# Kernel tuning notes

Measured on AMD Instinct MI355X. Metric: run time of the kernel, lower is better.

Reference implementation:

```python
import jax, jax.numpy as jnp
import numpy as np

EPS = 1e-12  # torch F.normalize eps

def _l2norm(t):
    # normalize over last axis (tokens N), matching F.normalize(dim=-1)
    n = jnp.sqrt(jnp.sum(t * t, axis=-1, keepdims=True))
    return t / jnp.maximum(n, EPS)

def setup_inputs() -> dict:
    key = jax.random.key(0)
    ks = jax.random.split(key, 4)
    B, N, C, H = 16, 3136, 768, 16
    x = jax.random.normal(ks[0], (B, N, C), dtype=jnp.float32)
    w_qkv = jax.random.normal(ks[1], (3 * C, C), dtype=jnp.float32) * (C ** -0.5)
    temperature = jnp.ones((H, 1, 1), dtype=jnp.float32)
    w_proj = jax.random.normal(ks[2], (C, C), dtype=jnp.float32) * (C ** -0.5)
    b_proj = jnp.zeros((C,), dtype=jnp.float32)
    return {"x": x, "w_qkv": w_qkv, "temperature": temperature,
            "w_proj": w_proj, "b_proj": b_proj}

def reference(x, w_qkv, temperature, w_proj, b_proj):
    B, N, C = x.shape
    H = temperature.shape[0]
    dh = C // H
    # qkv: [B,N,3C] -> [B,N,3,H,dh] -> [3,B,H,dh,N]
    qkv = (x @ w_qkv.T).reshape(B, N, 3, H, dh)
    qkv = jnp.transpose(qkv, (2, 0, 3, 4, 1))
    q, k, v = qkv[0], qkv[1], qkv[2]          # each [B,H,dh,N]
    q = _l2norm(q)
    k = _l2norm(k)
    # cross-covariance attention over channel axis: [B,H,dh,dh]
    attn = jnp.einsum('bhdn,bhen->bhde', q, k) * temperature
    attn = jax.nn.softmax(attn, axis=-1)
    out = jnp.einsum('bhde,bhen->bhdn', attn, v)  # [B,H,dh,N]
    out = jnp.transpose(out, (0, 3, 1, 2)).reshape(B, N, C)
    return out @ w_proj.T + b_proj
```

## Files before the change

kernel.cpp:

```cpp
#include <hip/hip_runtime.h>
#include <hip/hip_bf16.h>
#include <stdint.h>

using f32x4   = __attribute__((ext_vector_type(4))) float;
using half8   = __attribute__((ext_vector_type(8))) _Float16;
using half4   = __attribute__((ext_vector_type(4))) _Float16;
using half2v  = __attribute__((ext_vector_type(2))) _Float16;
using float4v = __attribute__((ext_vector_type(4))) float;

typedef const __attribute__((address_space(1))) void gas_void;
typedef __attribute__((address_space(3))) void las_void;

__device__ __forceinline__ void gload_lds16(const void* gptr, void* lptr) {
  __builtin_amdgcn_global_load_lds((gas_void*)(uintptr_t)gptr,
                                   (las_void*)(uintptr_t)lptr, 16, 0, 0);
}

#define MFMA_F16(a, b, c) __builtin_amdgcn_mfma_f32_16x16x32_f16((a), (b), (c), 0, 0, 0)

__global__ __launch_bounds__(256)
void k_cvtx(const float* __restrict__ x, _Float16* __restrict__ x16,
            _Float16* __restrict__ xT,
            const float* __restrict__ wqkv, const float* __restrict__ wproj,
            _Float16* __restrict__ w16, _Float16* __restrict__ wp16,
            _Float16* __restrict__ wvT) {
  const int bid = blockIdx.x;
  if (bid >= 9408) {
    const long N1 = 221184L, N2 = 73728L, N3 = 98304L;
    const long total = N1 + N2 + N3;
    for (long i = (long)(bid - 9408) * blockDim.x + threadIdx.x; i < total;
         i += 512L * blockDim.x) {
      if (i < N1 + N2) {
        const float* src; _Float16* dst; long off;
        if (i < N1) { src = wqkv;  dst = w16;  off = i; }
        else        { src = wproj; dst = wp16; off = i - N1; }
        const float4v* p = (const float4v*)(src + off * 8);
        float4v a = p[0], b = p[1];
        half8 o;
        o[0] = (_Float16)a[0]; o[1] = (_Float16)a[1]; o[2] = (_Float16)a[2]; o[3] = (_Float16)a[3];
        o[4] = (_Float16)b[0]; o[5] = (_Float16)b[1]; o[6] = (_Float16)b[2]; o[7] = (_Float16)b[3];
        *(half8*)(dst + off * 8) = o;
      } else {
        const long u = i - N1 - N2;
        const int h = (int)(u / 6144);
        const int r = (int)(u % 6144);
        const int f = r >> 3, e0 = (r & 7) * 8;
        half8 o;
        if (e0 >= 48) {
#pragma unroll
          for (int j = 0; j < 8; ++j) o[j] = (_Float16)0.f;
        } else {
#pragma unroll
          for (int j = 0; j < 8; ++j)
            o[j] = (_Float16)wqkv[(long)(1536 + h * 48 + e0 + j) * 768 + f];
        }
        *(half8*)(wvT + ((long)(h * 768 + f) * 64 + e0)) = o;
      }
    }
    return;
  }
  __shared__ _Float16 lt[64 * 66];
  const int b = bid / 588;
  const int rem = bid % 588;
  const int tt = rem / 12, ct = rem % 12;
  const long t0g = (long)b * 3136 + tt * 64;
  const int c0 = ct * 64;
  const int tid = threadIdx.x;
#pragma unroll
  for (int ch = 0; ch < 4; ++ch) {
    const int idx = tid + ch * 256;
    const int tr = idx >> 4, cg = (idx & 15) * 4;
    float4v v = *(const float4v*)&x[(t0g + tr) * 768 + c0 + cg];
    half4 hv;
    hv[0] = (_Float16)v[0]; hv[1] = (_Float16)v[1];
    hv[2] = (_Float16)v[2]; hv[3] = (_Float16)v[3];
    *(half4*)&x16[(t0g + tr) * 768 + c0 + cg] = hv;
    half2v lo, hi;
    lo[0] = hv[0]; lo[1] = hv[1]; hi[0] = hv[2]; hi[1] = hv[3];
    *(half2v*)&lt[tr * 66 + cg]     = lo;
    *(half2v*)&lt[tr * 66 + cg + 2] = hi;
  }
  __syncthreads();
  const int c = tid >> 2, tch = tid & 3;
  half8 o0, o1;
#pragma unroll
  for (int j = 0; j < 8; ++j) o0[j] = lt[(tch * 16 + j) * 66 + c];
#pragma unroll
  for (int j = 0; j < 8; ++j) o1[j] = lt[(tch * 16 + 8 + j) * 66 + c];
  _Float16* dst = xT + (long)b * 2408448 + (long)(c0 + c) * 3136 + tt * 64 + tch * 16;
  *(half8*)dst = o0;
  *(half8*)(dst + 8) = o1;
}

__global__ __launch_bounds__(512)
void k_gram(const _Float16* __restrict__ xT, _Float16* __restrict__ G) {
  __shared__ _Float16 lds[2][2][128 * 64];
  const int tid = threadIdx.x;
  const int wv = tid >> 6, lane = tid & 63;
  const int g = lane >> 4, cidx = lane & 15;
  const int wr = wv >> 2, wc = wv & 3;

  const int nwg = (int)gridDim.x;
  const int q = nwg >> 3, r = nwg & 7;
  const int xcd = (int)blockIdx.x & 7, bidx = (int)blockIdx.x >> 3;
  int wg = (xcd < r ? xcd * (q + 1) : r * (q + 1) + (xcd - r) * q) + bidx;
  const int b = wg / 21;
  int p = wg % 21;
  int mt = 0;
  while (p >= 6 - mt) { p -= 6 - mt; ++mt; }
  const int nt = mt + p;

  const _Float16* Ab = xT + (long)b * 2408448 + (long)mt * 128 * 3136;
  const _Float16* Bb = xT + (long)b * 2408448 + (long)nt * 128 * 3136;

  const int srow8 = lane >> 3;
  const int sgr8  = (lane & 7) ^ srow8;

  auto stage = [&](int buf, int kt) {
#pragma unroll
    for (int l = 0; l < 2; ++l) {
      const int chunk = l * 8 + wv;
      const long grow = chunk * 8 + srow8;
      const long koff = (long)kt * 64 + sgr8 * 8;
      gload_lds16(Ab + grow * 3136 + koff, &lds[buf][0][chunk * 512]);
      gload_lds16(Bb + grow * 3136 + koff, &lds[buf][1][chunk * 512]);
    }
  };

  f32x4 acc[4][2] = {};
  stage(0, 0);
  __syncthreads();
  for (int kt = 0; kt < 49; ++kt) {
    const int cur = kt & 1;
    if (kt + 1 < 49) stage(cur ^ 1, kt + 1);
    half8 af[4][2], bf[2][2];
#pragma unroll
    for (int ks = 0; ks < 2; ++ks) {
      const int gran = (((ks << 2) + g) ^ (cidx & 7)) * 8;
#pragma unroll
      for (int m = 0; m < 4; ++m)
        af[m][ks] = *(const half8*)&lds[cur][0][(wr * 64 + m * 16 + cidx) * 64 + gran];
#pragma unroll
      for (int n = 0; n < 2; ++n)
        bf[n][ks] = *(const half8*)&lds[cur][1][(wc * 32 + n * 16 + cidx) * 64 + gran];
    }
#pragma unroll
    for (int ks = 0; ks < 2; ++ks)
#pragma unroll
      for (int m = 0; m < 4; ++m)
#pragma unroll
        for (int n = 0; n < 2; ++n)
          acc[m][n] = MFMA_F16(af[m][ks], bf[n][ks], acc[m][n]);
    __syncthreads();
  }
  _Float16* Gb = G + (long)b * 589824;
  const long m0 = (long)mt * 128, n0 = (long)nt * 128;
#pragma unroll
  for (int m = 0; m < 4; ++m)
#pragma unroll
    for (int rr = 0; rr < 4; ++rr) {
      const long row = m0 + wr * 64 + m * 16 + g * 4 + rr;
#pragma unroll
      for (int n = 0; n < 2; ++n)
        Gb[row * 768 + n0 + wc * 32 + n * 16 + cidx] = (_Float16)acc[m][n][rr];
    }
  if (mt != nt) {
#pragma unroll
    for (int m = 0; m < 4; ++m)
#pragma unroll
      for (int n = 0; n < 2; ++n) {
        half4 hv;
#pragma unroll
        for (int rr = 0; rr < 4; ++rr) hv[rr] = (_Float16)acc[m][n][rr];
        const long col  = n0 + wc * 32 + n * 16 + cidx;
        const long row0 = m0 + wr * 64 + m * 16 + g * 4;
        *(half4*)&Gb[col * 768 + row0] = hv;
      }
  }
}

#define XPH(CURA, CURB, MLO, NA, NBUF, NKS, NMLO, LOADB, NB, STAGE, BDRY)      \
  {                                                                            \
    STAGE;                                                                     \
    if (BDRY) {                                                                \
      asm volatile("s_waitcnt vmcnt(4)" ::: "memory");                         \
      __builtin_amdgcn_sched_barrier(0);                                       \
    }                                                                          \
    __builtin_amdgcn_s_barrier();                                              \
    _Pragma("unroll")                                                          \
    for (int mm = 0; mm < 4; ++mm)                                             \
      NA[mm] = *(const half8*)&lds[(NBUF)*32768 + (NKS)*8192 + raA + ((NMLO)+mm)*512]; \
    if (LOADB) {                                                               \
      _Pragma("unroll")                                                        \
      for (int nn = 0; nn < 4; ++nn)                                           \
        NB[nn] = *(const half8*)&lds[(NBUF)*32768 + (NKS)*8192 + raB + nn*512]; \
    }                                                                          \
    __builtin_amdgcn_sched_barrier(0);                                         \
    __builtin_amdgcn_s_setprio(1);                                             \
    _Pragma("unroll")                                                          \
    for (int mm = 0; mm < 4; ++mm)                                             \
      _Pragma("unroll")                                                        \
      for (int nn = 0; nn < 4; ++nn)                                           \
        acc[(MLO)+mm][nn] = MFMA_F16(CURA[mm], CURB[nn], acc[(MLO)+mm][nn]);   \
    __builtin_amdgcn_s_setprio(0);                                             \
    __builtin_amdgcn_s_barrier();                                              \
  }

template<bool OUT_F32>
__global__ __launch_bounds__(512, 2)
void k_gemm8p(const _Float16* __restrict__ A, const _Float16* __restrict__ B,
              void* __restrict__ Cv, const float* __restrict__ bias,
              int Mt, int Nt, long Areal, long Astr, long Bstr, long Cstr,
              long N, long K)
{
  __shared__ _Float16 lds[65536];
  const int tid  = threadIdx.x;
  const int wv   = tid >> 6, lane = tid & 63;
  const int g    = lane >> 4, cidx = lane & 15;
  const int wr   = wv >> 2, wc = wv & 3;

  const int nwg = (int)gridDim.x;
  const int q = nwg >> 3, r = nwg & 7;
  const int xcd = (int)blockIdx.x & 7, bidx = (int)blockIdx.x >> 3;
  int wg = (xcd < r ? xcd * (q + 1) : r * (q + 1) + (xcd - r) * q) + bidx;

  const int tpb = Mt * Nt;
  const int b   = wg / tpb;
  const int rem = wg - b * tpb;
  const long mt = rem % Mt, nt = rem / Mt;
  const long m0 = mt * 256, n0 = nt * 256;

  const int NT = (int)(K >> 6);
  const int NI = NT >> 1;

  const _Float16* Ab = A + b * Astr + m0 * K;
  const _Float16* Bb = B + b * Bstr + n0 * K;

  const int srow = lane >> 2;
  const int sgr  = (lane & 3) ^ ((lane >> 3) & 3);

  auto stage = [&](int op, int buf, int kh, int t) {
    const _Float16* src = op ? Bb : Ab;
    const long koff = (long)t * 64 + kh * 32 + sgr * 8;
#pragma unroll
    for (int l = 0; l < 2; ++l) {
      const int chunk = l * 8 + wv;
      gload_lds16(src + (long)(chunk * 16 + srow) * K + koff,
                  &lds[buf * 32768 + op * 16384 + kh * 8192 + chunk * 512]);
    }
  };

  const int gr  = (g ^ ((cidx >> 1) & 3)) * 8;
  const int raA = (wr * 128 + cidx) * 32 + gr;
  const int raB = 16384 + (wc * 64 + cidx) * 32 + gr;

  f32x4 acc[8][4] = {};

  stage(0, 0, 0, 0); stage(1, 0, 0, 0);
  stage(0, 0, 1, 0); stage(1, 0, 1, 0);
  stage(0, 1, 0, 1); stage(1, 1, 0, 1);
  asm volatile("s_waitcnt vmcnt(4)" ::: "memory");
  __builtin_amdgcn_sched_barrier(0);
  __builtin_amdgcn_s_barrier();

  half8 afA[4], afB[4], bfA[4], bfB[4];
#pragma unroll
  for (int mm = 0; mm < 4; ++mm) afA[mm] = *(const half8*)&lds[raA + mm * 512];
#pragma unroll
  for (int nn = 0; nn < 4; ++nn) bfA[nn] = *(const half8*)&lds[raB + nn * 512];

  for (int it = 0; it < NI; ++it) {
    const int t1c = 2 * it + 1;
    int tn2 = 2 * it + 2; if (tn2 >= NT) tn2 -= NT;
    int tn3 = 2 * it + 3; if (tn3 >= NT) tn3 -= NT;
    XPH(afA, bfA, 0, afB, 0, 0, 4, 0, bfB, stage(0, 1, 1, t1c), false)
    XPH(afB, bfA, 4, afA, 0, 1, 0, 1, bfB, stage(1, 1, 1, t1c), false)
    XPH(afA, bfB, 0, afB, 0, 1, 4, 0, bfA, stage(0, 0, 0, tn2), false)
    XPH(afB, bfB, 4, afA, 1, 0, 0, 1, bfA, stage(1, 0, 0, tn2), true )
    XPH(afA, bfA, 0, afB, 1, 0, 4, 0, bfB, stage(0, 0, 1, tn2), false)
    XPH(afB, bfA, 4, afA, 1, 1, 0, 1, bfB, stage(1, 0, 1, tn2), false)
    XPH(afA, bfB, 0, afB, 1, 1, 4, 0, bfA, stage(0, 1, 0, tn3), false)
    XPH(afB, bfB, 4, afA, 0, 0, 0, 1, bfA, stage(1, 1, 0, tn3), true )
  }

  float bv[4] = {0.f, 0.f, 0.f, 0.f};
  if (bias) {
#pragma unroll
    for (int n = 0; n < 4; ++n) bv[n] = bias[n0 + wc * 64 + n * 16 + cidx];
  }
  if constexpr (OUT_F32) {
    float* C = (float*)Cv + b * Cstr;
#pragma unroll
    for (int m = 0; m < 8; ++m)
#pragma unroll
      for (int rr = 0; rr < 4; ++rr) {
        const long row = m0 + wr * 128 + m * 16 + g * 4 + rr;
        if (row < Areal) {
#pragma unroll
          for (int n = 0; n < 4; ++n)
            C[row * N + (n0 + wc * 64 + n * 16 + cidx)] = acc[m][n][rr] + bv[n];
        }
      }
  } else {
    _Float16* C = (_Float16*)Cv + b * Cstr;
#pragma unroll
    for (int m = 0; m < 8; ++m)
#pragma unroll
      for (int rr = 0; rr < 4; ++rr) {
        const long row = m0 + wr * 128 + m * 16 + g * 4 + rr;
        if (row < Areal) {
#pragma unroll
          for (int n = 0; n < 4; ++n)
            C[row * N + (n0 + wc * 64 + n * 16 + cidx)] = (_Float16)acc[m][n][rr];
        }
      }
  }
}

#define XP3(CURA, CURB, MLO, NA, NSA, NKS, NMLO, LOADB, NB, NSB, STAGE, BDRY)  \
  {                                                                            \
    STAGE;                                                                     \
    if (BDRY) {                                                                \
      asm volatile("s_waitcnt vmcnt(4)" ::: "memory");                         \
      __builtin_amdgcn_sched_barrier(0);                                       \
    }                                                                          \
    __builtin_amdgcn_s_barrier();                                              \
    _Pragma("unroll")                                                          \
    for (int mm = 0; mm < 4; ++mm)                                             \
      NA[mm] = *(const half8*)&lds[(NSA)*16384 + ((raA + ((NMLO)+mm)*1024) ^ ((NKS)*32))]; \
    if (LOADB) {                                                               \
      _Pragma("unroll")                                                        \
      for (int nn = 0; nn < 4; ++nn)                                           \
        NB[nn] = *(const half8*)&lds[49152 + (NSB)*16384 + ((raB + nn*1024) ^ ((NKS)*32))]; \
    }                                                                          \
    __builtin_amdgcn_sched_barrier(0);                                         \
    __builtin_amdgcn_s_setprio(1);                                             \
    _Pragma("unroll")                                                          \
    for (int mm = 0; mm < 4; ++mm)                                             \
      _Pragma("unroll")                                                        \
      for (int nn = 0; nn < 4; ++nn)                                           \
        acc[(MLO)+mm][nn] = MFMA_F16(CURA[mm], CURB[nn], acc[(MLO)+mm][nn]);   \
    __builtin_amdgcn_s_setprio(0);                                             \
    __builtin_amdgcn_s_barrier();                                              \
  }

__global__ __launch_bounds__(512, 1)
void k_final3(const _Float16* __restrict__ A, const _Float16* __restrict__ B,
              float* __restrict__ C, const float* __restrict__ bias)
{
  __shared__ _Float16 lds[81920];
  const int tid = threadIdx.x;
  const int wv = tid >> 6, lane = tid & 63;
  const int g = lane >> 4, cidx = lane & 15;
  const int wr = wv >> 2, wc = wv & 3;
  const long K = 768;

  const int nwg = (int)gridDim.x;
  const int q = nwg >> 3, r = nwg & 7;
  const int xcd = (int)blockIdx.x & 7, bidx = (int)blockIdx.x >> 3;
  int wg = (xcd < r ? xcd * (q + 1) : r * (q + 1) + (xcd - r) * q) + bidx;
  const int b = wg / 39;
  const int rem = wg - b * 39;
  const long mt = rem % 13, nt = rem / 13;
  const long m0 = mt * 256, n0 = nt * 256;

  const _Float16* Ab = A + (long)b * 2408448 + m0 * K;
  const _Float16* Bb = B + (long)b * 589824 + n0 * K;

  const int srow8 = lane >> 3;
  const int sgr8  = (lane & 7) ^ srow8;

  auto stageA = [&](int slot, int t, int part) {
#pragma unroll
    for (int l = part * 2; l < part * 2 + 2; ++l) {
      const int chunk = l * 8 + wv;
      gload_lds16(Ab + (long)(chunk * 8 + srow8) * K + (long)t * 64 + sgr8 * 8,
                  &lds[slot * 16384 + chunk * 512]);
    }
  };
  auto stageB = [&](int slot, int t, int part) {
#pragma unroll
    for (int l = part * 2; l < part * 2 + 2; ++l) {
      const int chunk = l * 8 + wv;
      gload_lds16(Bb + (long)(chunk * 8 + srow8) * K + (long)t * 64 + sgr8 * 8,
                  &lds[49152 + slot * 16384 + chunk * 512]);
    }
  };

  const int gr0 = (g ^ (cidx & 7)) * 8;
  const int raA = (wr * 128 + cidx) * 64 + gr0;
  const int raB = (wc * 64 + cidx) * 64 + gr0;

  f32x4 acc[8][4] = {};

  stageA(0, 0, 0); stageA(0, 0, 1);
  stageB(0, 0, 0); stageB(0, 0, 1);
  stageA(1, 1, 0); stageA(1, 1, 1);
  asm volatile("s_waitcnt vmcnt(4)" ::: "memory");
  __builtin_amdgcn_sched_barrier(0);
  __builtin_amdgcn_s_barrier();

  half8 afA[4], afB[4], bfA[4], bfB[4];
#pragma unroll
  for (int mm = 0; mm < 4; ++mm)
    afA[mm] = *(const half8*)&lds[raA + mm * 1024];
#pragma unroll
  for (int nn = 0; nn < 4; ++nn)
    bfA[nn] = *(const half8*)&lds[49152 + raB + nn * 1024];

  int sa = 0, sb = 0;
  for (int t = 0; t < 12; ++t) {
    const int san  = (sa == 2) ? 0 : sa + 1;
    const int sap2 = (san == 2) ? 0 : san + 1;
    const int sbn  = sb ^ 1;
    int tb1 = t + 1; if (tb1 >= 12) tb1 -= 12;
    int tb2 = t + 2; if (tb2 >= 12) tb2 -= 12;
    XP3(afA, bfA, 0, afB, sa, 0, 4, 0, bfB, 0, stageB(sbn, tb1, 0), false)
    XP3(afB, bfA, 4, afA, sa, 1, 0, 1, bfB, sb, stageB(sbn, tb1, 1), false)
    XP3(afA, bfB, 0, afB, sa, 1, 4, 0, bfA, 0, stageA(sap2, tb2, 0), false)
    XP3(afB, bfB, 4, afA, san, 0, 0, 1, bfA, sbn, stageA(sap2, tb2, 1), true)
    sa = san; sb = sbn;
  }

  float bv[4];
#pragma unroll
  for (int n = 0; n < 4; ++n) bv[n] = bias[n0 + wc * 64 + n * 16 + cidx];
  float* Cb = C + (long)b * 2408448;
#pragma unroll
  for (int m = 0; m < 8; ++m)
#pragma unroll
    for (int rr = 0; rr < 4; ++rr) {
      const long row = m0 + wr * 128 + m * 16 + g * 4 + rr;
      if (row < 3136) {
#pragma unroll
        for (int n = 0; n < 4; ++n)
          Cb[row * 768 + (n0 + wc * 64 + n * 16 + cidx)] = acc[m][n][rr] + bv[n];
      }
    }
}

__global__ __launch_bounds__(256)
void k_heads(const _Float16* __restrict__ QG, const _Float16* __restrict__ w16,
             const _Float16* __restrict__ wvT, const float* __restrict__ temperature,
             _Float16* __restrict__ weffT)
{
  const int b = blockIdx.x >> 4, h = blockIdx.x & 15;
  const int tid = threadIdx.x;
  const int w = tid >> 6, lane = tid & 63;
  const int g = lane >> 4, c = lane & 15;

  __shared__ float red[4][48 * 48];
  __shared__ float redss[4][2][48];
  __shared__ float inv[2][48];
  __shared__ _Float16 Pb[48 * 64];

  const _Float16* QGq = QG + (long)b * 1179648 + (long)(h * 48) * 768;
  const _Float16* QGk = QGq + 768L * 768;
  const _Float16* Wq  = w16 + (long)(h * 48) * 768;
  const _Float16* Wk  = w16 + (long)(768 + h * 48) * 768;

  f32x4 aS[3][3] = {};
  f32x4 aq[3] = {};
  f32x4 ak[3] = {};
  for (int ks = w * 6; ks < w * 6 + 6; ++ks) {
    const int k0 = ks * 32 + g * 8;
    half8 t1[3], t3[3], wqf[3], wkf[3];
#pragma unroll
    for (int m = 0; m < 3; ++m) {
      const long ro = (long)(m * 16 + c) * 768 + k0;
      t1[m]  = *(const half8*)(QGq + ro);
      t3[m]  = *(const half8*)(QGk + ro);
      wqf[m] = *(const half8*)(Wq + ro);
      wkf[m] = *(const half8*)(Wk + ro);
    }
#pragma unroll
    for (int m = 0; m < 3; ++m) {
      aq[m] = MFMA_F16(t1[m], wqf[m], aq[m]);
      ak[m] = MFMA_F16(t3[m], wkf[m], ak[m]);
#pragma unroll
      for (int n = 0; n < 3; ++n)
        aS[m][n] = MFMA_F16(t1[m], wkf[n], aS[m][n]);
    }
  }

#pragma unroll
  for (int m = 0; m < 3; ++m) {
#pragma unroll
    for (int n = 0; n < 3; ++n)
#pragma unroll
      for (int rr = 0; rr < 4; ++rr)
        red[w][(m * 16 + g * 4 + rr) * 48 + n * 16 + c] = aS[m][n][rr];
#pragma unroll
    for (int rr = 0; rr < 4; ++rr)
      if (c == g * 4 + rr) {
        redss[w][0][m * 16 + c] = aq[m][rr];
        redss[w][1][m * 16 + c] = ak[m][rr];
      }
  }
  __syncthreads();

  if (tid < 96) {
    const int is_k = tid / 48, d = tid % 48;
    const float s = redss[0][is_k][d] + redss[1][is_k][d] + redss[2][is_k][d] + redss[3][is_k][d];
    inv[is_k][d] = 1.0f / fmaxf(sqrtf(s), 1e-12f);
  }
  __syncthreads();

  if (tid < 48) {
    const int d = tid;
    const float iq = inv[0][d] * temperature[h];
    float rowv[48];
    float mx = -3.0e38f;
#pragma unroll
    for (int e = 0; e < 48; ++e) {
      const int idx = d * 48 + e;
      float t = (red[0][idx] + red[1][idx] + red[2][idx] + red[3][idx]) * iq * inv[1][e];
      rowv[e] = t;
      mx = fmaxf(mx, t);
    }
    float sum = 0.f;
#pragma unroll
    for (int e = 0; e < 48; ++e) {
      const float pv = __expf(rowv[e] - mx);
      rowv[e] = pv;
      sum += pv;
    }
    const float is = 1.0f / sum;
#pragma unroll
    for (int e = 0; e < 48; ++e)
      Pb[d * 64 + e] = (_Float16)(rowv[e] * is);
#pragma unroll
    for (int e = 48; e < 64; ++e)
      Pb[d * 64 + e] = (_Float16)0.f;
  }
  __syncthreads();

  half8 pf[3][2];
#pragma unroll
  for (int nf = 0; nf < 3; ++nf)
#pragma unroll
    for (int ks = 0; ks < 2; ++ks)
      pf[nf][ks] = *(const half8*)&Pb[(nf * 16 + c) * 64 + ks * 32 + g * 8];

  const _Float16* wvh = wvT + (long)h * 768 * 64;
  _Float16* wout = weffT + (long)b * 589824 + h * 48;

  for (int m = 0; m < 12; ++m) {
    const int f0 = w * 192 + m * 16;
    half8 va[2];
#pragma unroll
    for (int ks = 0; ks < 2; ++ks)
      va[ks] = *(const half8*)&wvh[(long)(f0 + c) * 64 + ks * 32 + g * 8];
    f32x4 a3[3] = {};
#pragma unroll
    for (int ks = 0; ks < 2; ++ks)
#pragma unroll
      for (int nf = 0; nf < 3; ++nf)
        a3[nf] = MFMA_F16(va[ks], pf[nf][ks], a3[nf]);
#pragma unroll
    for (int nf = 0; nf < 3; ++nf)
#pragma unroll
      for (int rr = 0; rr < 4; ++rr)
        wout[(long)(f0 + g * 4 + rr) * 768 + nf * 16 + c] = (_Float16)a3[nf][rr];
  }
}

extern "C" void kernel_launch(void* const* d_in, const int* in_sizes, int n_in,
                              void* d_out, int out_size, void* d_ws, size_t ws_size,
                              hipStream_t stream)
{
  (void)in_sizes; (void)n_in; (void)out_size; (void)ws_size;
  const float* x      = (const float*)d_in[0];
  const float* w_qkv  = (const float*)d_in[1];
  const float* temp   = (const float*)d_in[2];
  const float* w_proj = (const float*)d_in[3];
  const float* b_proj = (const float*)d_in[4];
  float* out = (float*)d_out;

  char* ws = (char*)d_ws;
  _Float16* x16   = (_Float16*)(ws);
  _Float16* xT    = (_Float16*)(ws + 77070336L);
  _Float16* G     = (_Float16*)(ws + 154140672L);
  _Float16* QG    = (_Float16*)(ws + 173015040L);
  _Float16* weffT = (_Float16*)(ws + 210763776L);
  _Float16* wfin  = (_Float16*)(ws + 229638144L);
  _Float16* w16   = (_Float16*)(ws + 248512512L);
  _Float16* wp16  = (_Float16*)(ws + 252051456L);
  _Float16* wvT   = (_Float16*)(ws + 253231104L);

  k_cvtx<<<9920, 256, 0, stream>>>(x, x16, xT, w_qkv, w_proj, w16, wp16, wvT);
  k_gram<<<336, 512, 0, stream>>>(xT, G);
  k_gemm8p<false><<<288, 512, 0, stream>>>(w16, G, QG, nullptr,
                                           6, 3, 1536, 0, 589824, 1179648, 768, 768);
  k_heads<<<256, 256, 0, stream>>>(QG, w16, wvT, temp, weffT);
  k_gemm8p<false><<<144, 512, 0, stream>>>(wp16, weffT, wfin, nullptr,
                                           3, 3, 768, 0, 589824, 589824, 768, 768);
  k_final3<<<624, 512, 0, stream>>>(x16, wfin, out, b_proj);
}
```

Baseline: 314.7 us.

## Shrink final GEMM M tile to 128 and reuse generic kernel for QG GEMM

Replaces the 256x256-tile final GEMM with a templated 128x256-tile kernel that uses a two-phase pipeline per K step and less LDS. The same kernel now also replaces the QG projection GEMM, doubling its grid. The aim is more workgroups and better CU occupancy and tail balance, since the 624- and 288-block grids left CUs underused. In exchange each tile reuses B data less and issues more global loads per FLOP.

```diff
diff --git a/kernel.cpp b/kernel.cpp
--- a/kernel.cpp
+++ b/kernel.cpp
@@ -317,38 +317,38 @@
   }
 }
 
-#define XP3(CURA, CURB, MLO, NA, NSA, NKS, NMLO, LOADB, NB, NSB, STAGE, BDRY)  \
+#define XP2(CURA, CURB, NA, NSA, NB, NSB, NKS, STAGE, BDRY)                    \
   {                                                                            \
     STAGE;                                                                     \
     if (BDRY) {                                                                \
-      asm volatile("s_waitcnt vmcnt(4)" ::: "memory");                         \
+      asm volatile("s_waitcnt vmcnt(2)" ::: "memory");                         \
       __builtin_amdgcn_sched_barrier(0);                                       \
     }                                                                          \
     __builtin_amdgcn_s_barrier();                                              \
     _Pragma("unroll")                                                          \
     for (int mm = 0; mm < 4; ++mm)                                             \
-      NA[mm] = *(const half8*)&lds[(NSA)*16384 + ((raA + ((NMLO)+mm)*1024) ^ ((NKS)*32))]; \
-    if (LOADB) {                                                               \
-      _Pragma("unroll")                                                        \
-      for (int nn = 0; nn < 4; ++nn)                                           \
-        NB[nn] = *(const half8*)&lds[49152 + (NSB)*16384 + ((raB + nn*1024) ^ ((NKS)*32))]; \
-    }                                                                          \
+      NA[mm] = *(const half8*)&lds[(NSA)*8192 + ((raA + mm*1024) ^ ((NKS)*32))]; \
+    _Pragma("unroll")                                                          \
+    for (int nn = 0; nn < 4; ++nn)                                             \
+      NB[nn] = *(const half8*)&lds[24576 + (NSB)*16384 + ((raB + nn*1024) ^ ((NKS)*32))]; \
     __builtin_amdgcn_sched_barrier(0);                                         \
     __builtin_amdgcn_s_setprio(1);                                             \
     _Pragma("unroll")                                                          \
     for (int mm = 0; mm < 4; ++mm)                                             \
       _Pragma("unroll")                                                        \
       for (int nn = 0; nn < 4; ++nn)                                           \
-        acc[(MLO)+mm][nn] = MFMA_F16(CURA[mm], CURB[nn], acc[(MLO)+mm][nn]);   \
+        acc[mm][nn] = MFMA_F16(CURA[mm], CURB[nn], acc[mm][nn]);               \
     __builtin_amdgcn_s_setprio(0);                                             \
     __builtin_amdgcn_s_barrier();                                              \
   }
 
+template<bool OUT_F32>
 __global__ __launch_bounds__(512, 1)
-void k_final3(const _Float16* __restrict__ A, const _Float16* __restrict__ B,
-              float* __restrict__ C, const float* __restrict__ bias)
+void k_g2t(const _Float16* __restrict__ A, const _Float16* __restrict__ B,
+           void* __restrict__ Cv, const float* __restrict__ bias,
+           int Mt, int Nt, long Areal, long Astr, long Bstr, long Cstr, long N)
 {
-  __shared__ _Float16 lds[81920];
+  __shared__ _Float16 lds[57344];
   const int tid = threadIdx.x;
   const int wv = tid >> 6, lane = tid & 63;
   const int g = lane >> 4, cidx = lane & 15;
@@ -359,54 +359,53 @@
   const int q = nwg >> 3, r = nwg & 7;
   const int xcd = (int)blockIdx.x & 7, bidx = (int)blockIdx.x >> 3;
   int wg = (xcd < r ? xcd * (q + 1) : r * (q + 1) + (xcd - r) * q) + bidx;
-  const int b = wg / 39;
-  const int rem = wg - b * 39;
-  const long mt = rem % 13, nt = rem / 13;
-  const long m0 = mt * 256, n0 = nt * 256;
-
-  const _Float16* Ab = A + (long)b * 2408448 + m0 * K;
-  const _Float16* Bb = B + (long)b * 589824 + n0 * K;
+  const int tpb = Mt * Nt;
+  const int b = wg / tpb;
+  const int rem = wg - b * tpb;
+  const long mt = rem % Mt, nt = rem / Mt;
+  const long m0 = mt * 128, n0 = nt * 256;
+
+  const _Float16* Ab = A + b * Astr + m0 * K;
+  const _Float16* Bb = B + b * Bstr + n0 * K;
 
   const int srow8 = lane >> 3;
   const int sgr8  = (lane & 7) ^ srow8;
 
-  auto stageA = [&](int slot, int t, int part) {
-#pragma unroll
-    for (int l = part * 2; l < part * 2 + 2; ++l) {
+  auto stageA = [&](int slot, int t) {
+#pragma unroll
+    for (int l = 0; l < 2; ++l) {
       const int chunk = l * 8 + wv;
       gload_lds16(Ab + (long)(chunk * 8 + srow8) * K + (long)t * 64 + sgr8 * 8,
-                  &lds[slot * 16384 + chunk * 512]);
+                  &lds[slot * 8192 + chunk * 512]);
     }
   };
-  auto stageB = [&](int slot, int t, int part) {
-#pragma unroll
-    for (int l = part * 2; l < part * 2 + 2; ++l) {
+  auto stageB = [&](int slot, int t) {
+#pragma unroll
+    for (int l = 0; l < 4; ++l) {
       const int chunk = l * 8 + wv;
       gload_lds16(Bb + (long)(chunk * 8 + srow8) * K + (long)t * 64 + sgr8 * 8,
-                  &lds[49152 + slot * 16384 + chunk * 512]);
+                  &lds[24576 + slot * 16384 + chunk * 512]);
     }
   };
 
   const int gr0 = (g ^ (cidx & 7)) * 8;
-  const int raA = (wr * 128 + cidx) * 64 + gr0;
+  const int raA = (wr * 64 + cidx) * 64 + gr0;
   const int raB = (wc * 64 + cidx) * 64 + gr0;
 
-  f32x4 acc[8][4] = {};
-
-  stageA(0, 0, 0); stageA(0, 0, 1);
-  stageB(0, 0, 0); stageB(0, 0, 1);
-  stageA(1, 1, 0); stageA(1, 1, 1);
-  asm volatile("s_waitcnt vmcnt(4)" ::: "memory");
+  f32x4 acc[4][4] = {};
+
+  stageA(0, 0);
+  stageB(0, 0);
+  stageA(1, 1);
+  asm volatile("s_waitcnt vmcnt(2)" ::: "memory");
   __builtin_amdgcn_sched_barrier(0);
   __builtin_amdgcn_s_barrier();
 
   half8 afA[4], afB[4], bfA[4], bfB[4];
 #pragma unroll
-  for (int mm = 0; mm < 4; ++mm)
-    afA[mm] = *(const half8*)&lds[raA + mm * 1024];
-#pragma unroll
-  for (int nn = 0; nn < 4; ++nn)
-    bfA[nn] = *(const half8*)&lds[49152 + raB + nn * 1024];
+  for (int mm = 0; mm < 4; ++mm) afA[mm] = *(const half8*)&lds[raA + mm * 1024];
+#pragma unroll
+  for (int nn = 0; nn < 4; ++nn) bfA[nn] = *(const half8*)&lds[24576 + raB + nn * 1024];
 
   int sa = 0, sb = 0;
   for (int t = 0; t < 12; ++t) {
@@ -415,28 +414,43 @@
     const int sbn  = sb ^ 1;
     int tb1 = t + 1; if (tb1 >= 12) tb1 -= 12;
     int tb2 = t + 2; if (tb2 >= 12) tb2 -= 12;
-    XP3(afA, bfA, 0, afB, sa, 0, 4, 0, bfB, 0, stageB(sbn, tb1, 0), false)
-    XP3(afB, bfA, 4, afA, sa, 1, 0, 1, bfB, sb, stageB(sbn, tb1, 1), false)
-    XP3(afA, bfB, 0, afB, sa, 1, 4, 0, bfA, 0, stageA(sap2, tb2, 0), false)
-    XP3(afB, bfB, 4, afA, san, 0, 0, 1, bfA, sbn, stageA(sap2, tb2, 1), true)
+    XP2(afA, bfA, afB, sa, bfB, sb, 1, stageB(sbn, tb1), false)
+    XP2(afB, bfB, afA, san, bfA, sbn, 0, stageA(sap2, tb2), true)
     sa = san; sb = sbn;
   }
 
-  float bv[4];
-#pragma unroll
-  for (int n = 0; n < 4; ++n) bv[n] = bias[n0 + wc * 64 + n * 16 + cidx];
-  float* Cb = C + (long)b * 2408448;
-#pragma unroll
-  for (int m = 0; m < 8; ++m)
-#pragma unroll
-    for (int rr = 0; rr < 4; ++rr) {
-      const long row = m0 + wr * 128 + m * 16 + g * 4 + rr;
-      if (row < 3136) {
-#pragma unroll
-        for (int n = 0; n < 4; ++n)
-          Cb[row * 768 + (n0 + wc * 64 + n * 16 + cidx)] = acc[m][n][rr] + bv[n];
+  float bv[4] = {0.f, 0.f, 0.f, 0.f};
+  if (bias) {
+#pragma unroll
+    for (int n = 0; n < 4; ++n) bv[n] = bias[n0 + wc * 64 + n * 16 + cidx];
+  }
+  if constexpr (OUT_F32) {
+    float* C = (float*)Cv + b * Cstr;
+#pragma unroll
+    for (int m = 0; m < 4; ++m)
+#pragma unroll
+      for (int rr = 0; rr < 4; ++rr) {
+        const long row = m0 + wr * 64 + m * 16 + g * 4 + rr;
+        if (row < Areal) {
+#pragma unroll
+          for (int n = 0; n < 4; ++n)
+            C[row * N + (n0 + wc * 64 + n * 16 + cidx)] = acc[m][n][rr] + bv[n];
+        }
       }
-    }
+  } else {
+    _Float16* C = (_Float16*)Cv + b * Cstr;
+#pragma unroll
+    for (int m = 0; m < 4; ++m)
+#pragma unroll
+      for (int rr = 0; rr < 4; ++rr) {
+        const long row = m0 + wr * 64 + m * 16 + g * 4 + rr;
+        if (row < Areal) {
+#pragma unroll
+          for (int n = 0; n < 4; ++n)
+            C[row * N + (n0 + wc * 64 + n * 16 + cidx)] = (_Float16)acc[m][n][rr];
+        }
+      }
+  }
 }
 
 __global__ __launch_bounds__(256)
@@ -590,10 +604,11 @@
 
   k_cvtx<<<9920, 256, 0, stream>>>(x, x16, xT, w_qkv, w_proj, w16, wp16, wvT);
   k_gram<<<336, 512, 0, stream>>>(xT, G);
-  k_gemm8p<false><<<288, 512, 0, stream>>>(w16, G, QG, nullptr,
-                                           6, 3, 1536, 0, 589824, 1179648, 768, 768);
+  k_g2t<false><<<576, 512, 0, stream>>>(w16, G, QG, nullptr,
+                                        12, 3, 1536, 0, 589824, 1179648, 768);
   k_heads<<<256, 256, 0, stream>>>(QG, w16, wvT, temp, weffT);
   k_gemm8p<false><<<144, 512, 0, stream>>>(wp16, weffT, wfin, nullptr,
                                            3, 3, 768, 0, 589824, 589824, 768, 768);
-  k_final3<<<624, 512, 0, stream>>>(x16, wfin, out, b_proj);
+  k_g2t<true><<<1200, 512, 0, stream>>>(x16, wfin, out, b_proj,
+                                        25, 3, 3136, 2408448, 589824, 2408448, 768);
 }
```

After: 321.0 us. 1.02x slower.
